# Performance work log

Measured on AMD Instinct MI355X. Metric: run time of the kernel, lower is better.

Reference implementation:

```python
import jax, jax.numpy as jnp
import numpy as np
from jax import lax

B, C, H, W, NH = 16, 512, 32, 32, 8
HC = C // NH  # head channels = 64


def setup_inputs() -> dict:
    key = jax.random.key(0)
    ks = jax.random.split(key, 8)
    rn = lambda i, shape, scale: jax.random.normal(ks[i], shape, jnp.float32) * scale
    return dict(
        image=jax.random.normal(ks[0], (B, C, H, W), jnp.float32),
        watermark=jax.random.normal(ks[1], (B, C, H, W), jnp.float32),
        img_ln_w=jnp.ones((C, H, W), jnp.float32),
        img_ln_b=jnp.zeros((C, H, W), jnp.float32),
        wm_ln_w=jnp.ones((C, H, W), jnp.float32),
        wm_ln_b=jnp.zeros((C, H, W), jnp.float32),
        img_pw_w=rn(2, (3 * C, C), 0.02),
        img_pw_b=jnp.zeros((3 * C,), jnp.float32),
        img_dw_w=rn(3, (3 * C, 3, 3, 3), 0.1),
        img_dw_b=jnp.zeros((3 * C,), jnp.float32),
        wm_pw_w=rn(4, (3 * C, C), 0.02),
        wm_pw_b=jnp.zeros((3 * C,), jnp.float32),
        wm_dw_w=rn(5, (3 * C, 3, 3, 3), 0.1),
        wm_dw_b=jnp.zeros((3 * C,), jnp.float32),
        proj=rn(6, (2 * C, C), 0.02),
    )


def _layernorm(x, w, b, eps=1e-5):
    # LayerNorm over [C,H,W] per sample, elementwise affine of shape [C,H,W]
    mu = jnp.mean(x, axis=(1, 2, 3), keepdims=True)
    var = jnp.mean((x - mu) ** 2, axis=(1, 2, 3), keepdims=True)
    return (x - mu) * lax.rsqrt(var + eps) * w + b


def _dconv_proj(x, pw_w, pw_b, dw_w, dw_b):
    # pointwise 1x1 conv C -> 3C
    x = jnp.einsum('bchw,oc->bohw', x, pw_w) + pw_b[None, :, None, None]
    # depthwise 3x3 conv on 3C channels with groups=C (3 channels per group)
    x = lax.conv_general_dilated(
        x, dw_w, window_strides=(1, 1), padding='SAME',
        dimension_numbers=('NCHW', 'OIHW', 'NCHW'), feature_group_count=C)
    x = x + dw_b[None, :, None, None]
    return jnp.split(x, 3, axis=1)  # Q, K, V each [B,C,H,W]


def reference(image, watermark, img_ln_w, img_ln_b, wm_ln_w, wm_ln_b,
              img_pw_w, img_pw_b, img_dw_w, img_dw_b,
              wm_pw_w, wm_pw_b, wm_dw_w, wm_dw_b, proj):
    img = _layernorm(image, img_ln_w, img_ln_b)
    wm = _layernorm(watermark, wm_ln_w, wm_ln_b)
    Qi, Ki, Vi = _dconv_proj(img, img_pw_w, img_pw_b, img_dw_w, img_dw_b)
    Qw, Kw, Vw = _dconv_proj(wm, wm_pw_w, wm_pw_b, wm_dw_w, wm_dw_b)
    r = lambda t: t.reshape(B, NH, HC, H * W)
    Qi, Ki, Vi, Qw, Kw, Vw = map(r, (Qi, Ki, Vi, Qw, Kw, Vw))
    # NOTE: original code calls F.normalize but discards the result -> no-op.
    Kc = jnp.concatenate([Ki, Kw], axis=2)  # [B,NH,2*HC,HW]
    Vc = jnp.concatenate([Vi, Vw], axis=2)  # [B,NH,2*HC,HW]
    # scores: K_concat @ Q^T over the HW axis -> [B,NH,2*HC,HC], softmax over HC
    Ai = jax.nn.softmax(jnp.einsum('bnkp,bnqp->bnkq', Kc, Qi), axis=-1)
    Aw = jax.nn.softmax(jnp.einsum('bnkp,bnqp->bnkq', Kc, Qw), axis=-1)
    # A^T @ V_concat -> [B,NH,HC,HW]
    img_attn = jnp.einsum('bnkq,bnkp->bnqp', Ai, Vc)
    wm_attn = jnp.einsum('bnkq,bnkp->bnqp', Aw, Vc)
    attn = jnp.concatenate([img_attn, wm_attn], axis=2).reshape(B, 2 * C, H, W)
    # final channel-mixing projection: [B,H,W,2C] @ [2C,C] -> [B,C,H,W]
    return jnp.einsum('bdhw,dc->bchw', attn, proj)
```

## Files before the change

### kernel.cpp

```cpp
#include <hip/hip_runtime.h>
#include <hip/hip_bf16.h>
#include <stdint.h>

#define Bn  16
#define Cch 512
#define C3  1536
#define HWp 1024

typedef __attribute__((ext_vector_type(8))) short bf16x8;
typedef __attribute__((ext_vector_type(4))) float f32x4;

#define DEV static __device__ __forceinline__

DEV float bflo(unsigned u) { return __builtin_bit_cast(float, u << 16); }
DEV float bfhi(unsigned u) { return __builtin_bit_cast(float, u & 0xffff0000u); }
DEV unsigned short f2bf(float f) {
  __hip_bfloat16 h = __float2bfloat16(f);
  return __builtin_bit_cast(unsigned short, h);
}

DEV void async16(__hip_bfloat16* lds, const __hip_bfloat16* g) {
  __builtin_amdgcn_global_load_lds(
      (const __attribute__((address_space(1))) unsigned*)g,
      (__attribute__((address_space(3))) unsigned*)lds, 16, 0, 0);
}

__global__ __launch_bounds__(256) void k_prep_ln(
    const float* __restrict__ img_pw_w, const float* __restrict__ wm_pw_w,
    const float* __restrict__ proj,
    const float* __restrict__ image, const float* __restrict__ watermark,
    __hip_bfloat16* __restrict__ Wpw, __hip_bfloat16* __restrict__ projT,
    float* __restrict__ part)
{
  __shared__ float ls[4], lss[4];
  int blkid = blockIdx.x;
  if (blkid < 8192) {
    int i = blkid * 256 + threadIdx.x;
    const int NW = C3 * Cch;
    if (i < NW)          Wpw[i] = __float2bfloat16(img_pw_w[i]);
    else if (i < 2 * NW) Wpw[i] = __float2bfloat16(wm_pw_w[i - NW]);
    else {
      int j = i - 2 * NW;
      int c = j >> 10, d = j & 1023;
      projT[(size_t)c * 1024 + d] = __float2bfloat16(proj[(size_t)d * 512 + c]);
    }
    return;
  }
  int blk = blkid - 8192;
  int chunk = blk & 63, b = (blk >> 6) & 15, t = blk >> 10;
  const float* x = (t ? watermark : image) + (size_t)b * Cch * HWp + chunk * 8192;
  const float4* xv = (const float4*)x;
  float s = 0.f, ss = 0.f;
#pragma unroll
  for (int i = 0; i < 8; i++) {
    float4 v = xv[threadIdx.x + i * 256];
    s  += v.x + v.y + v.z + v.w;
    ss += v.x * v.x + v.y * v.y + v.z * v.z + v.w * v.w;
  }
#pragma unroll
  for (int off = 32; off; off >>= 1) { s += __shfl_down(s, off); ss += __shfl_down(ss, off); }
  int wv = threadIdx.x >> 6;
  if ((threadIdx.x & 63) == 0) { ls[wv] = s; lss[wv] = ss; }
  __syncthreads();
  if (threadIdx.x == 0) {
    part[blk * 2]     = ls[0] + ls[1] + ls[2] + ls[3];
    part[blk * 2 + 1] = lss[0] + lss[1] + lss[2] + lss[3];
  }
}

__global__ void k_ln_final(const float* __restrict__ part, float* __restrict__ stats)
{
  int i = threadIdx.x;
  if (i < 32) {
    float S = 0.f, SS = 0.f;
    for (int c2 = 0; c2 < 64; c2++) { S += part[(i * 64 + c2) * 2]; SS += part[(i * 64 + c2) * 2 + 1]; }
    const float inv = 1.f / (float)(Cch * HWp);
    float mu  = S * inv;
    float var = SS * inv - mu * mu;
    stats[i]      = mu;
    stats[32 + i] = rsqrtf(var + 1e-5f);
  }
}

__global__ __launch_bounds__(256) void k_norm_t(
    const float* __restrict__ image, const float* __restrict__ watermark,
    const float* __restrict__ img_w, const float* __restrict__ img_b,
    const float* __restrict__ wm_w,  const float* __restrict__ wm_b,
    const float* __restrict__ stats, __hip_bfloat16* __restrict__ xnT)
{
  int blk = blockIdx.x;
  int ct = blk & 15, pt = (blk >> 4) & 15, b = (blk >> 8) & 15, t = blk >> 12;
  int c0 = ct * 32, p0 = pt * 64;
  const float* x   = (t ? watermark : image) + (size_t)b * Cch * HWp;
  const float* wgt = t ? wm_w : img_w;
  const float* bia = t ? wm_b : img_b;
  float mu = stats[t * 16 + b], rstd = stats[32 + t * 16 + b];
  __shared__ float tile[32 * 66];
  int tid = threadIdx.x;
  {
    int c = tid >> 3, s = tid & 7;
    const float* xr = x   + (size_t)(c0 + c) * HWp + p0;
    const float* wr = wgt + (size_t)(c0 + c) * HWp + p0;
    const float* br = bia + (size_t)(c0 + c) * HWp + p0;
#pragma unroll
    for (int j = 0; j < 2; j++) {
      int f = s + j * 8;
      float4 xv = *(const float4*)&xr[f * 4];
      float4 wv = *(const float4*)&wr[f * 4];
      float4 bv = *(const float4*)&br[f * 4];
      float n0 = (xv.x - mu) * rstd * wv.x + bv.x;
      float n1 = (xv.y - mu) * rstd * wv.y + bv.y;
      float n2 = (xv.z - mu) * rstd * wv.z + bv.z;
      float n3 = (xv.w - mu) * rstd * wv.w + bv.w;
      *(float2*)&tile[c * 66 + f * 4]     = make_float2(n0, n1);
      *(float2*)&tile[c * 66 + f * 4 + 2] = make_float2(n2, n3);
    }
  }
  __syncthreads();
  {
    int p = tid >> 2, cq = tid & 3;
    union { unsigned short us[8]; uint4 v4; } pk;
#pragma unroll
    for (int j = 0; j < 8; j++) pk.us[j] = f2bf(tile[(cq * 8 + j) * 66 + p]);
    __hip_bfloat16* dst = xnT + ((size_t)(t * 16 + b)) * HWp * Cch
                        + (size_t)(p0 + p) * Cch + c0 + cq * 8;
    *(uint4*)dst = pk.v4;
  }
}

template<int MI, int Kdim, int Ncols, bool OBF, bool HB>
DEV void gemm_core(const __hip_bfloat16* __restrict__ A,
                   const __hip_bfloat16* __restrict__ Bt,
                   const float* __restrict__ bias, void* __restrict__ Cout)
{
  constexpr int MT = MI * 32;
  __shared__ __hip_bfloat16 As[MT * 64];
  __shared__ __hip_bfloat16 Bs[128 * 64];
  const int tid = threadIdx.x, lane = tid & 63, wv = tid >> 6;
  const int lr = lane & 15, lq = lane >> 4;
  const int wm = (wv >> 1) * (MI * 16), wn = (wv & 1) * 64;
  const int m0 = blockIdx.y * MT, n0 = blockIdx.x * 128;
  f32x4 acc[MI][4] = {};
  const int srow = tid >> 3, sslot = tid & 7;
  const int sseg = (sslot ^ (srow & 7)) * 8;
  for (int k0 = 0; k0 < Kdim; k0 += 64) {
#pragma unroll
    for (int c = 0; c < MI; c++) {
      int row = srow + c * 32;
      async16(&As[row * 64 + sslot * 8], &A[(size_t)(m0 + row) * Kdim + k0 + sseg]);
    }
#pragma unroll
    for (int c = 0; c < 4; c++) {
      int row = srow + c * 32;
      async16(&Bs[row * 64 + sslot * 8], &Bt[(size_t)(n0 + row) * Kdim + k0 + sseg]);
    }
    __syncthreads();
#pragma unroll
    for (int ks = 0; ks < 2; ks++) {
      bf16x8 af[MI], bfr[4];
#pragma unroll
      for (int mi = 0; mi < MI; mi++) {
        int r = wm + mi * 16 + lr;
        af[mi]  = *(const bf16x8*)&As[r * 64 + (((ks * 4 + lq) ^ (lr & 7)) * 8)];
      }
#pragma unroll
      for (int ni = 0; ni < 4; ni++) {
        int r = wn + ni * 16 + lr;
        bfr[ni] = *(const bf16x8*)&Bs[r * 64 + (((ks * 4 + lq) ^ (lr & 7)) * 8)];
      }
#pragma unroll
      for (int mi = 0; mi < MI; mi++)
#pragma unroll
        for (int ni = 0; ni < 4; ni++)
          acc[mi][ni] = __builtin_amdgcn_mfma_f32_16x16x32_bf16(af[mi], bfr[ni], acc[mi][ni], 0, 0, 0);
    }
    __syncthreads();
  }
#pragma unroll
  for (int mi = 0; mi < MI; mi++) {
    int mrow = m0 + wm + mi * 16 + lq * 4;
#pragma unroll
    for (int ni = 0; ni < 4; ni++) {
      int ncol = n0 + wn + ni * 16 + lr;
#pragma unroll
      for (int r = 0; r < 4; r++) {
        float y = acc[mi][ni][r];
        int row = mrow + r;
        if (HB) y += bias[row];
        if (OBF) ((__hip_bfloat16*)Cout)[(size_t)row * Ncols + ncol] = __float2bfloat16(y);
        else     ((float*)Cout)[(size_t)row * Ncols + ncol] = y;
      }
    }
  }
}

__global__ __launch_bounds__(512) void k_pw_gemm256(
    const __hip_bfloat16* __restrict__ Wpw, const __hip_bfloat16* __restrict__ xnT,
    const float* __restrict__ img_pw_b, const float* __restrict__ wm_pw_b,
    __hip_bfloat16* __restrict__ Y)
{
  constexpr int K = 512, NT = K / 64;
  __shared__ __hip_bfloat16 lds[2][2][256 * 64];
  const int bz = blockIdx.z, t = bz >> 4;
  const __hip_bfloat16* Ag = Wpw + (size_t)t * C3 * Cch;
  const __hip_bfloat16* Bg = xnT + (size_t)bz * HWp * Cch;
  const float* bias = t ? wm_pw_b : img_pw_b;
  __hip_bfloat16* Co = Y + (size_t)bz * C3 * HWp;
  const int m0 = blockIdx.y * 256, n0 = blockIdx.x * 256;
  const int tid = threadIdx.x, lane = tid & 63, wv = tid >> 6;
  const int lr = lane & 15, lq = lane >> 4;
  const int wm = (wv >> 2) * 128, wn = (wv & 3) * 64;
  const int srow = tid >> 3, sslot = tid & 7;
  const int sseg = (sslot ^ (srow & 7)) * 8;
  f32x4 acc[8][4] = {};

  auto stage = [&](int kt) {
    const int p = kt & 1;
    const __hip_bfloat16* Ak = Ag + (size_t)(m0 + srow) * K + kt * 64 + sseg;
    const __hip_bfloat16* Bk = Bg + (size_t)(n0 + srow) * K + kt * 64 + sseg;
    __hip_bfloat16* La = &lds[p][0][srow * 64 + sslot * 8];
    __hip_bfloat16* Lb = &lds[p][1][srow * 64 + sslot * 8];
#pragma unroll
    for (int c = 0; c < 4; c++) {
      async16(La + c * 64 * 64, Ak + (size_t)c * 64 * K);
      async16(Lb + c * 64 * 64, Bk + (size_t)c * 64 * K);
    }
  };

  stage(0);
  stage(1);
  for (int kt = 0; kt < NT; ++kt) {
    if (kt < NT - 1) asm volatile("s_waitcnt vmcnt(8)" ::: "memory");
    else             asm volatile("s_waitcnt vmcnt(0)" ::: "memory");
    __builtin_amdgcn_s_barrier();
    __builtin_amdgcn_sched_barrier(0);
    const int p = kt & 1;
    const __hip_bfloat16* As = lds[p][0];
    const __hip_bfloat16* Bs = lds[p][1];
    bf16x8 af[2][8], bfr[2][4];
#pragma unroll
    for (int ks = 0; ks < 2; ks++) {
#pragma unroll
      for (int mi = 0; mi < 8; mi++) {
        int r = wm + mi * 16 + lr;
        af[ks][mi] = *(const bf16x8*)&As[r * 64 + (((ks * 4 + lq) ^ (lr & 7)) * 8)];
      }
#pragma unroll
      for (int ni = 0; ni < 4; ni++) {
        int r = wn + ni * 16 + lr;
        bfr[ks][ni] = *(const bf16x8*)&Bs[r * 64 + (((ks * 4 + lq) ^ (lr & 7)) * 8)];
      }
    }
    __builtin_amdgcn_s_setprio(1);
#pragma unroll
    for (int mi = 0; mi < 8; mi++)
#pragma unroll
      for (int ni = 0; ni < 4; ni++)
        acc[mi][ni] = __builtin_amdgcn_mfma_f32_16x16x32_bf16(af[0][mi], bfr[0][ni], acc[mi][ni], 0, 0, 0);
    __builtin_amdgcn_s_setprio(0);
    asm volatile("s_waitcnt lgkmcnt(0)" ::: "memory");
    __builtin_amdgcn_sched_barrier(0);
    __builtin_amdgcn_s_barrier();
    __builtin_amdgcn_sched_barrier(0);
    if (kt + 2 < NT) stage(kt + 2);
    __builtin_amdgcn_s_setprio(1);
#pragma unroll
    for (int mi = 0; mi < 8; mi++)
#pragma unroll
      for (int ni = 0; ni < 4; ni++)
        acc[mi][ni] = __builtin_amdgcn_mfma_f32_16x16x32_bf16(af[1][mi], bfr[1][ni], acc[mi][ni], 0, 0, 0);
    __builtin_amdgcn_s_setprio(0);
  }
#pragma unroll
  for (int mi = 0; mi < 8; mi++) {
    int mrow = m0 + wm + mi * 16 + lq * 4;
#pragma unroll
    for (int ni = 0; ni < 4; ni++) {
      int ncol = n0 + wn + ni * 16 + lr;
#pragma unroll
      for (int r = 0; r < 4; r++) {
        float y = acc[mi][ni][r] + bias[mrow + r];
        Co[(size_t)(mrow + r) * HWp + ncol] = __float2bfloat16(y);
      }
    }
  }
}

__global__ __launch_bounds__(256) void k_proj_gemm(
    const __hip_bfloat16* __restrict__ projT, const __hip_bfloat16* __restrict__ attnT,
    float* __restrict__ out)
{
  int b = blockIdx.z;
  gemm_core<4, 1024, 1024, false, false>(
      projT, attnT + (size_t)b * HWp * 1024, nullptr, out + (size_t)b * Cch * HWp);
}

__global__ __launch_bounds__(256) void k_dw(
    const __hip_bfloat16* __restrict__ Y,
    const float* __restrict__ img_dw_w, const float* __restrict__ img_dw_b,
    const float* __restrict__ wm_dw_w,  const float* __restrict__ wm_dw_b,
    __hip_bfloat16* __restrict__ QKV)
{
  int idx = blockIdx.x * 256 + threadIdx.x;
  int w0 = (idx & 3) * 8;
  int h  = (idx >> 2) & 31;
  int g  = __builtin_amdgcn_readfirstlane((idx >> 7) & 511);
  int tb = __builtin_amdgcn_readfirstlane(idx >> 16);
  int t  = tb >> 4;
  const float* dww = (t ? wm_dw_w : img_dw_w) + g * 81;
  const float* dwb = (t ? wm_dw_b : img_dw_b) + g * 3;
  const __hip_bfloat16* base = Y + ((size_t)tb * C3 + g * 3) * HWp;
  float acc[3][8];
#pragma unroll
  for (int o = 0; o < 3; o++) {
    float bv = dwb[o];
#pragma unroll
    for (int w = 0; w < 8; w++) acc[o][w] = bv;
  }
  const bool mlo = (w0 == 0), mhi = (w0 == 24);
#pragma unroll
  for (int i = 0; i < 3; i++) {
#pragma unroll
    for (int kh = 0; kh < 3; kh++) {
      int hh = h + kh - 1;
      if ((unsigned)hh > 31u) continue;
      const unsigned* up = (const unsigned*)(base + i * HWp + hh * 32 + (w0 - 2));
      float v[12];
#pragma unroll
      for (int d2 = 0; d2 < 6; d2++) { unsigned u = up[d2]; v[d2*2] = bflo(u); v[d2*2+1] = bfhi(u); }
      if (mlo) { v[0] = 0.f; v[1] = 0.f; }
      if (mhi) { v[10] = 0.f; v[11] = 0.f; }
#pragma unroll
      for (int o = 0; o < 3; o++) {
        float wk0 = dww[o*27 + i*9 + kh*3 + 0];
        float wk1 = dww[o*27 + i*9 + kh*3 + 1];
        float wk2 = dww[o*27 + i*9 + kh*3 + 2];
#pragma unroll
        for (int w = 0; w < 8; w++)
          acc[o][w] += v[w + 1] * wk0 + v[w + 2] * wk1 + v[w + 3] * wk2;
      }
    }
  }
#pragma unroll
  for (int o = 0; o < 3; o++) {
    union { unsigned short us[8]; uint4 v4; } pk;
#pragma unroll
    for (int w = 0; w < 8; w++) pk.us[w] = f2bf(acc[o][w]);
    *(uint4*)(QKV + ((size_t)tb * C3 + g * 3 + o) * HWp + h * 32 + w0) = pk.v4;
  }
}

__global__ __launch_bounds__(256) void k_attn_scores(
    const __hip_bfloat16* __restrict__ QKV, __hip_bfloat16* __restrict__ ATg)
{
  int blk = blockIdx.x, kh = blk & 1, m = (blk >> 1) & 1, bn = blk >> 2;
  int b = bn >> 3, nh = bn & 7;
  int tid = threadIdx.x, lane = tid & 63, wv = tid >> 6;
  int lr = lane & 15, lq = lane >> 4;
  const __hip_bfloat16* kb =
      QKV + (((size_t)(kh * 16 + b)) * C3 + 512 + nh * 64 + (wv * 16 + lr)) * HWp + lq * 8;
  const __hip_bfloat16* qbase[4];
#pragma unroll
  for (int qt = 0; qt < 4; qt++)
    qbase[qt] = QKV + (((size_t)(m * 16 + b)) * C3 + nh * 64 + qt * 16 + lr) * HWp + lq * 8;

  f32x4 acc[4] = {};
  for (int p0 = 0; p0 < HWp; p0 += 32) {
    bf16x8 bk = *(const bf16x8*)(kb + p0);
#pragma unroll
    for (int qt = 0; qt < 4; qt++) {
      bf16x8 aq = *(const bf16x8*)(qbase[qt] + p0);
      acc[qt] = __builtin_amdgcn_mfma_f32_16x16x32_bf16(aq, bk, acc[qt], 0, 0, 0);
    }
  }
  __shared__ float S[64][65];
  __shared__ float redmax[4][64];
  __shared__ float redsum[4][64];
  __shared__ __hip_bfloat16 Ash[64][72];
#pragma unroll
  for (int qt = 0; qt < 4; qt++)
#pragma unroll
    for (int r = 0; r < 4; r++)
      S[qt * 16 + lq * 4 + r][wv * 16 + lr] = acc[qt][r];
  __syncthreads();
  int k = tid & 63, sub = tid >> 6;
  float vals[16], mx = -1e30f;
#pragma unroll
  for (int j = 0; j < 16; j++) { vals[j] = S[sub * 16 + j][k]; mx = fmaxf(mx, vals[j]); }
  redmax[sub][k] = mx;
  __syncthreads();
  float M = fmaxf(fmaxf(redmax[0][k], redmax[1][k]), fmaxf(redmax[2][k], redmax[3][k]));
  float ssum = 0.f;
#pragma unroll
  for (int j = 0; j < 16; j++) { vals[j] = __expf(vals[j] - M); ssum += vals[j]; }
  redsum[sub][k] = ssum;
  __syncthreads();
  float inv = 1.f / (redsum[0][k] + redsum[1][k] + redsum[2][k] + redsum[3][k]);
#pragma unroll
  for (int j = 0; j < 16; j++) Ash[sub * 16 + j][k] = __float2bfloat16(vals[j] * inv);
  __syncthreads();
  __hip_bfloat16* outp = ATg + ((size_t)(bn * 2 + m)) * 64 * 128 + kh * 64;
#pragma unroll
  for (int s = 0; s < 2; s++) {
    int id = tid + s * 256, row = id >> 3, seg = (id & 7) * 8;
    *(uint4*)&outp[(size_t)row * 128 + seg] = *(const uint4*)&Ash[row][seg];
  }
}

__global__ __launch_bounds__(256) void k_attn_out(
    const __hip_bfloat16* __restrict__ QKV, const __hip_bfloat16* __restrict__ ATg,
    __hip_bfloat16* __restrict__ attnT)
{
  int blk = blockIdx.x, pc = blk & 3, bn = blk >> 2, b = bn >> 3, nh = bn & 7;
  int tid = threadIdx.x, lane = tid & 63, wv = tid >> 6;
  int lr = lane & 15, lq = lane >> 4;
  __shared__ __hip_bfloat16 ATs[2][64][136];
  __shared__ __hip_bfloat16 VTs[64][136];
#pragma unroll
  for (int m = 0; m < 2; m++) {
    const __hip_bfloat16* src = ATg + ((size_t)(bn * 2 + m)) * 64 * 128;
#pragma unroll
    for (int s = 0; s < 4; s++) {
      int id = tid + s * 256, row = id >> 4, seg = (id & 15) * 8;
      *(uint4*)&ATs[m][row][seg] = *(const uint4*)&src[row * 128 + seg];
    }
  }
  const int vk0 = (tid >> 3) * 4, vps = (tid & 7) * 8;
  for (int ps = 0; ps < 4; ps++) {
    int p0 = pc * 256 + ps * 64;
    __syncthreads();
    union { uint4 v4; unsigned short us[8]; } ld[4];
#pragma unroll
    for (int j = 0; j < 4; j++) {
      int kk = vk0 + j, tk = kk >> 6, hc = kk & 63;
      ld[j].v4 = *(const uint4*)(QKV +
          (((size_t)(tk * 16 + b)) * C3 + 1024 + nh * 64 + hc) * HWp + p0 + vps);
    }
#pragma unroll
    for (int e = 0; e < 8; e++) {
      uint2 w;
      w.x = (unsigned)ld[0].us[e] | ((unsigned)ld[1].us[e] << 16);
      w.y = (unsigned)ld[2].us[e] | ((unsigned)ld[3].us[e] << 16);
      *(uint2*)&VTs[vps + e][vk0] = w;
    }
    __syncthreads();
#pragma unroll
    for (int m = 0; m < 2; m++) {
      f32x4 oacc[4] = {};
#pragma unroll
      for (int ks = 0; ks < 4; ks++) {
        bf16x8 bv = *(const bf16x8*)&VTs[wv * 16 + lr][ks * 32 + lq * 8];
#pragma unroll
        for (int qt = 0; qt < 4; qt++) {
          bf16x8 av = *(const bf16x8*)&ATs[m][qt * 16 + lr][ks * 32 + lq * 8];
          oacc[qt] = __builtin_amdgcn_mfma_f32_16x16x32_bf16(av, bv, oacc[qt], 0, 0, 0);
        }
      }
#pragma unroll
      for (int qt = 0; qt < 4; qt++) {
        int q = qt * 16 + lq * 4;
        int d = nh * 128 + m * 64 + q;
        int p = p0 + wv * 16 + lr;
        union { unsigned short us[4]; uint2 v2; } pk;
#pragma unroll
        for (int r = 0; r < 4; r++) pk.us[r] = f2bf(oacc[qt][r]);
        *(uint2*)&attnT[((size_t)b * HWp + p) * 1024 + d] = pk.v2;
      }
    }
  }
}

extern "C" void kernel_launch(void* const* d_in, const int* in_sizes, int n_in,
                              void* d_out, int out_size, void* d_ws, size_t ws_size,
                              hipStream_t stream)
{
  (void)in_sizes; (void)n_in; (void)out_size; (void)ws_size;
  const float* image     = (const float*)d_in[0];
  const float* watermark = (const float*)d_in[1];
  const float* img_ln_w  = (const float*)d_in[2];
  const float* img_ln_b  = (const float*)d_in[3];
  const float* wm_ln_w   = (const float*)d_in[4];
  const float* wm_ln_b   = (const float*)d_in[5];
  const float* img_pw_w  = (const float*)d_in[6];
  const float* img_pw_b  = (const float*)d_in[7];
  const float* img_dw_w  = (const float*)d_in[8];
  const float* img_dw_b  = (const float*)d_in[9];
  const float* wm_pw_w   = (const float*)d_in[10];
  const float* wm_pw_b   = (const float*)d_in[11];
  const float* wm_dw_w   = (const float*)d_in[12];
  const float* wm_dw_b   = (const float*)d_in[13];
  const float* proj      = (const float*)d_in[14];

  char* ws = (char*)d_ws;
  __hip_bfloat16* Wpw    = (__hip_bfloat16*)(ws + 0);
  __hip_bfloat16* projT  = (__hip_bfloat16*)(ws + 3145728);
  float*          lnpart = (float*)(ws + 4194304);
  float*          stats  = (float*)(ws + 4210688);
  __hip_bfloat16* xnT    = (__hip_bfloat16*)(ws + 5242880);
  __hip_bfloat16* attnT  = xnT;
  __hip_bfloat16* Y      = (__hip_bfloat16*)(ws + 41943040);
  __hip_bfloat16* ATg    = Y;
  __hip_bfloat16* QKV    = (__hip_bfloat16*)(ws + 142606336);

  k_prep_ln<<<10240, 256, 0, stream>>>(img_pw_w, wm_pw_w, proj, image, watermark,
                                       Wpw, projT, lnpart);
  k_ln_final<<<1, 64, 0, stream>>>(lnpart, stats);
  k_norm_t<<<8192, 256, 0, stream>>>(image, watermark, img_ln_w, img_ln_b,
                                     wm_ln_w, wm_ln_b, stats, xnT);
  dim3 gpw(4, 6, 32);
  k_pw_gemm256<<<gpw, 512, 0, stream>>>(Wpw, xnT, img_pw_b, wm_pw_b, Y);
  k_dw<<<8192, 256, 0, stream>>>(Y, img_dw_w, img_dw_b, wm_dw_w, wm_dw_b, QKV);
  k_attn_scores<<<512, 256, 0, stream>>>(QKV, ATg);
  k_attn_out<<<512, 256, 0, stream>>>(QKV, ATg, attnT);
  dim3 gpj(8, 4, 16);
  k_proj_gemm<<<gpj, 256, 0, stream>>>(projT, attnT, (float*)d_out);
}
```

Before: 381.9 us.

## Restructure pointwise GEMM into fine-grained ping-pong phases with split-half LDS staging

Rewrites the main loop of the 256x256 pointwise-conv GEMM into eight barrier-separated phases per two k-tiles. Each phase interleaves LDS fragment reads, quarter-sized MFMA blocks and async global-to-LDS loads of half-tiles, so memory traffic overlaps compute at a finer grain and fewer fragment registers are live. It also sets launch_bounds min-blocks to 2 to cap register use. The risks are many more barriers per tile and possible register spills under the tighter bound.

```diff
diff --git a/kernel.cpp b/kernel.cpp
--- a/kernel.cpp
+++ b/kernel.cpp
@@ -194,13 +194,14 @@
   }
 }
 
-__global__ __launch_bounds__(512) void k_pw_gemm256(
+__global__ __launch_bounds__(512, 2) void k_pw_gemm256(
     const __hip_bfloat16* __restrict__ Wpw, const __hip_bfloat16* __restrict__ xnT,
     const float* __restrict__ img_pw_b, const float* __restrict__ wm_pw_b,
     __hip_bfloat16* __restrict__ Y)
 {
-  constexpr int K = 512, NT = K / 64;
-  __shared__ __hip_bfloat16 lds[2][2][256 * 64];
+  constexpr int K = 512, NT = 8;
+  __shared__ __hip_bfloat16 LA[2][2][128 * 64];
+  __shared__ __hip_bfloat16 LB[2][2][128 * 64];
   const int bz = blockIdx.z, t = bz >> 4;
   const __hip_bfloat16* Ag = Wpw + (size_t)t * C3 * Cch;
   const __hip_bfloat16* Bg = xnT + (size_t)bz * HWp * Cch;
@@ -210,67 +211,94 @@
   const int tid = threadIdx.x, lane = tid & 63, wv = tid >> 6;
   const int lr = lane & 15, lq = lane >> 4;
   const int wm = (wv >> 2) * 128, wn = (wv & 3) * 64;
+  const int ah = wm >> 7;
+  const int bh = wn >> 7, bro = wn & 64;
   const int srow = tid >> 3, sslot = tid & 7;
   const int sseg = (sslot ^ (srow & 7)) * 8;
   f32x4 acc[8][4] = {};
-
-  auto stage = [&](int kt) {
-    const int p = kt & 1;
-    const __hip_bfloat16* Ak = Ag + (size_t)(m0 + srow) * K + kt * 64 + sseg;
-    const __hip_bfloat16* Bk = Bg + (size_t)(n0 + srow) * K + kt * 64 + sseg;
-    __hip_bfloat16* La = &lds[p][0][srow * 64 + sslot * 8];
-    __hip_bfloat16* Lb = &lds[p][1][srow * 64 + sslot * 8];
-#pragma unroll
-    for (int c = 0; c < 4; c++) {
-      async16(La + c * 64 * 64, Ak + (size_t)c * 64 * K);
-      async16(Lb + c * 64 * 64, Bk + (size_t)c * 64 * K);
-    }
+  bf16x8 af[8], bfr[2][4];
+
+  auto stageA = [&](int p, int h, int kt) {
+    const __hip_bfloat16* src = Ag + (size_t)(m0 + h * 128 + srow) * K + kt * 64 + sseg;
+    __hip_bfloat16* dst = &LA[p][h][srow * 64 + sslot * 8];
+    async16(dst, src);
+    async16(dst + 64 * 64, src + (size_t)64 * K);
   };
-
-  stage(0);
-  stage(1);
-  for (int kt = 0; kt < NT; ++kt) {
-    if (kt < NT - 1) asm volatile("s_waitcnt vmcnt(8)" ::: "memory");
-    else             asm volatile("s_waitcnt vmcnt(0)" ::: "memory");
-    __builtin_amdgcn_s_barrier();
-    __builtin_amdgcn_sched_barrier(0);
-    const int p = kt & 1;
-    const __hip_bfloat16* As = lds[p][0];
-    const __hip_bfloat16* Bs = lds[p][1];
-    bf16x8 af[2][8], bfr[2][4];
-#pragma unroll
-    for (int ks = 0; ks < 2; ks++) {
-#pragma unroll
-      for (int mi = 0; mi < 8; mi++) {
-        int r = wm + mi * 16 + lr;
-        af[ks][mi] = *(const bf16x8*)&As[r * 64 + (((ks * 4 + lq) ^ (lr & 7)) * 8)];
-      }
-#pragma unroll
-      for (int ni = 0; ni < 4; ni++) {
-        int r = wn + ni * 16 + lr;
-        bfr[ks][ni] = *(const bf16x8*)&Bs[r * 64 + (((ks * 4 + lq) ^ (lr & 7)) * 8)];
-      }
-    }
+  auto stageB = [&](int p, int h, int kt) {
+    const __hip_bfloat16* src = Bg + (size_t)(n0 + h * 128 + srow) * K + kt * 64 + sseg;
+    __hip_bfloat16* dst = &LB[p][h][srow * 64 + sslot * 8];
+    async16(dst, src);
+    async16(dst + 64 * 64, src + (size_t)64 * K);
+  };
+  auto readA = [&](int p, int ks) {
+#pragma unroll
+    for (int mi = 0; mi < 8; mi++)
+      af[mi] = *(const bf16x8*)&LA[p][ah][(mi * 16 + lr) * 64 + (((ks * 4 + lq) ^ (lr & 7)) * 8)];
+  };
+  auto readB4 = [&](int p, int nh) {
+#pragma unroll
+    for (int ks = 0; ks < 2; ks++)
+#pragma unroll
+      for (int ni = 0; ni < 2; ni++) {
+        int r = bro + (nh * 2 + ni) * 16 + lr;
+        bfr[ks][nh * 2 + ni] =
+            *(const bf16x8*)&LB[p][bh][r * 64 + (((ks * 4 + lq) ^ (lr & 7)) * 8)];
+      }
+  };
+  auto mma16 = [&](int ks, int nh) {
     __builtin_amdgcn_s_setprio(1);
 #pragma unroll
     for (int mi = 0; mi < 8; mi++)
 #pragma unroll
-      for (int ni = 0; ni < 4; ni++)
-        acc[mi][ni] = __builtin_amdgcn_mfma_f32_16x16x32_bf16(af[0][mi], bfr[0][ni], acc[mi][ni], 0, 0, 0);
+      for (int ni = 0; ni < 2; ni++)
+        acc[mi][nh * 2 + ni] = __builtin_amdgcn_mfma_f32_16x16x32_bf16(
+            af[mi], bfr[ks][nh * 2 + ni], acc[mi][nh * 2 + ni], 0, 0, 0);
     __builtin_amdgcn_s_setprio(0);
-    asm volatile("s_waitcnt lgkmcnt(0)" ::: "memory");
-    __builtin_amdgcn_sched_barrier(0);
-    __builtin_amdgcn_s_barrier();
-    __builtin_amdgcn_sched_barrier(0);
-    if (kt + 2 < NT) stage(kt + 2);
-    __builtin_amdgcn_s_setprio(1);
-#pragma unroll
-    for (int mi = 0; mi < 8; mi++)
-#pragma unroll
-      for (int ni = 0; ni < 4; ni++)
-        acc[mi][ni] = __builtin_amdgcn_mfma_f32_16x16x32_bf16(af[1][mi], bfr[1][ni], acc[mi][ni], 0, 0, 0);
-    __builtin_amdgcn_s_setprio(0);
-  }
+  };
+
+#define PH_MID  do { __builtin_amdgcn_sched_barrier(0); __builtin_amdgcn_s_barrier(); \
+                     asm volatile("s_waitcnt lgkmcnt(0)" ::: "memory");               \
+                     __builtin_amdgcn_sched_barrier(0); } while (0)
+#define PH_END  do { __builtin_amdgcn_sched_barrier(0); __builtin_amdgcn_s_barrier(); } while (0)
+
+  stageB(0, 0, 0); stageB(0, 1, 0); stageA(0, 0, 0); stageA(0, 1, 0);
+  stageB(1, 0, 1); stageB(1, 1, 1); stageA(1, 0, 1);
+  asm volatile("s_waitcnt vmcnt(6)" ::: "memory");
+  __builtin_amdgcn_sched_barrier(0);
+  __builtin_amdgcn_s_barrier();
+
+  for (int it = 0; it < NT / 2; ++it) {
+    const int v = 2 * it + 1, w = 2 * it + 2, x = 2 * it + 3;
+    const bool haveW = (w < NT), haveX = (x < NT), lastIt = (it == NT / 2 - 1);
+    readA(0, 0); readB4(0, 0);
+    stageA(1, 1, v);
+    PH_MID; mma16(0, 0); PH_END;
+    readB4(0, 1);
+    PH_MID; mma16(0, 1); PH_END;
+    readA(0, 1);
+    if (haveW) stageB(0, 0, w);
+    PH_MID; mma16(1, 0); PH_END;
+    if (haveW) { stageB(0, 1, w); stageA(0, 0, w); }
+    PH_MID; mma16(1, 1);
+    if (lastIt) asm volatile("s_waitcnt vmcnt(0)" ::: "memory");
+    else        asm volatile("s_waitcnt vmcnt(6)" ::: "memory");
+    PH_END;
+    readA(1, 0); readB4(1, 0);
+    if (haveW) stageA(0, 1, w);
+    PH_MID; mma16(0, 0); PH_END;
+    readB4(1, 1);
+    PH_MID; mma16(0, 1); PH_END;
+    readA(1, 1);
+    if (haveX) stageB(1, 0, x);
+    PH_MID; mma16(1, 0); PH_END;
+    if (haveX) { stageB(1, 1, x); stageA(1, 0, x); }
+    PH_MID; mma16(1, 1);
+    if (!lastIt) asm volatile("s_waitcnt vmcnt(6)" ::: "memory");
+    PH_END;
+  }
+#undef PH_MID
+#undef PH_END
+
 #pragma unroll
   for (int mi = 0; mi < 8; mi++) {
     int mrow = m0 + wm + mi * 16 + lq * 4;
```

New measurement: 384.3 us. About the same (+0.6%).
